# Optimization experiments

Hardware: AMD Instinct MI355X
Metric: run time of the kernel (lower is better)

## Reference

```python
import jax, jax.numpy as jnp
import numpy as np
from math import log2, floor

B, N, DIM = 2, 2048, 2048
HEADS, DIM_HEAD, FF_MULT = 16, 128, 4
RMS_EPS = 1e-8


def _get_slopes(heads):
    def pow2_slopes(n):
        start = 2 ** (-2 ** (-(log2(n) - 3)))
        return [start * start ** i for i in range(n)]
    if log2(heads).is_integer():
        return pow2_slopes(heads)
    closest = 2 ** floor(log2(heads))
    return pow2_slopes(closest) + pow2_slopes(2 * closest)[0::2][: heads - closest]


def setup_inputs() -> dict:
    key = jax.random.key(0)
    ks = jax.random.split(key, 5)
    std = 0.02
    return {
        "x": jax.random.normal(ks[0], (B, N, DIM), dtype=jnp.float32),
        "g": jnp.ones((DIM,), dtype=jnp.float32),
        "w_qkv": jax.random.normal(ks[1], (DIM, DIM + DIM_HEAD), dtype=jnp.float32) * std,
        "w_attn_out": jax.random.normal(ks[2], (DIM, DIM), dtype=jnp.float32) * std,
        "w_ff1": jax.random.normal(ks[3], (DIM, 2 * FF_MULT * DIM), dtype=jnp.float32) * std,
        "w_ff2": jax.random.normal(ks[4], (FF_MULT * DIM, DIM), dtype=jnp.float32) * std,
    }


def reference(x, g, w_qkv, w_attn_out, w_ff1, w_ff2):
    b, n, dim = x.shape
    # RMSNorm: x / clamp(||x|| * dim^-0.5, eps) * g
    norm = jnp.linalg.norm(x, axis=-1, keepdims=True) * (dim ** -0.5)
    xn = x / jnp.maximum(norm, RMS_EPS) * g

    # Parallel SwiGLU FFN branch (shares normed input with attention)
    h = xn @ w_ff1                       # [b, n, 2*ff_mult*dim]
    val, gate = jnp.split(h, 2, axis=-1)
    ff_out = (jax.nn.silu(gate) * val) @ w_ff2  # [b, n, dim]

    # Multi-query attention: single dim_head-wide kv shared as K and V
    qkv = xn @ w_qkv                     # [b, n, dim + dim_head]
    q, kv = qkv[..., :dim], qkv[..., dim:]
    q = q.reshape(b, n, HEADS, DIM_HEAD) * (DIM_HEAD ** -0.5)
    sim = jnp.einsum('bihd,bjd->bhij', q, kv)  # [b, h, n, n]

    # ALiBi bias: -|j - i| * slope_h
    slopes = jnp.asarray(_get_slopes(HEADS), dtype=sim.dtype)[:, None, None]
    pos = jnp.arange(n)
    bias = -jnp.abs(pos[None, None, :] - pos[None, :, None]).astype(sim.dtype) * slopes
    sim = sim + bias

    # Causal mask (strict upper triangle masked)
    causal = jnp.triu(jnp.ones((n, n), dtype=bool), 1)
    neg = jnp.asarray(jnp.finfo(sim.dtype).max, sim.dtype)
    sim = jnp.where(causal, -neg, sim)

    attn = jax.nn.softmax(sim, axis=-1)
    out = jnp.einsum('bhij,bjd->bhid', attn, kv)     # [b, h, n, dim_head]
    out = out.transpose(0, 2, 1, 3).reshape(b, n, dim)
    return out @ w_attn_out + ff_out
```

## Files before the change

kernel.cpp:

```cpp
#include <hip/hip_runtime.h>
#include <stdint.h>

typedef unsigned short u16;
typedef __attribute__((ext_vector_type(8))) short bf16x8;
typedef __attribute__((ext_vector_type(4))) float f32x4;
typedef __attribute__((ext_vector_type(8))) unsigned short us8;
typedef __attribute__((ext_vector_type(4))) float fvec4;

#define BATCH 2
#define SEQ   2048
#define DIMM  2048
#define NH    16
#define DH    128
#define ROWS  (BATCH*SEQ)
#define QKVN  (DIMM + DH)
#define FFH   8192
#define LOG2E 1.44269504088896340736f

static __device__ __forceinline__ u16 f2bf(float x) {
  union { float f; uint32_t u; } v; v.f = x;
  uint32_t r = (v.u + 0x7fffu + ((v.u >> 16) & 1u)) >> 16;
  return (u16)r;
}

static __device__ __forceinline__ float fast_exp2(float x) {
  float r; asm("v_exp_f32 %0, %1" : "=v"(r) : "v"(x)); return r;
}

static __device__ __forceinline__ void gld_lds16(const void* g, void* l) {
  __builtin_amdgcn_global_load_lds(
      (const __attribute__((address_space(1))) uint32_t*)g,
      (__attribute__((address_space(3))) uint32_t*)l, 16, 0, 0);
}

__global__ __launch_bounds__(256)
void rmsnorm_k(const float* __restrict__ x, const float* __restrict__ g, u16* __restrict__ xn) {
  const int row = blockIdx.x;
  const float* xr = x + (size_t)row * DIMM;
  const int off = threadIdx.x * 8;
  fvec4 a = *(const fvec4*)(xr + off);
  fvec4 b = *(const fvec4*)(xr + off + 4);
  float ss = a[0]*a[0]+a[1]*a[1]+a[2]*a[2]+a[3]*a[3]
           + b[0]*b[0]+b[1]*b[1]+b[2]*b[2]+b[3]*b[3];
  #pragma unroll
  for (int m = 32; m >= 1; m >>= 1) ss += __shfl_xor(ss, m);
  __shared__ float red[4];
  if ((threadIdx.x & 63) == 0) red[threadIdx.x >> 6] = ss;
  __syncthreads();
  float tot = red[0] + red[1] + red[2] + red[3];
  float inv = 1.0f / fmaxf(sqrtf(tot * (1.0f / DIMM)), 1e-8f);
  fvec4 ga = *(const fvec4*)(g + off);
  fvec4 gb = *(const fvec4*)(g + off + 4);
  us8 o;
  #pragma unroll
  for (int i = 0; i < 4; i++) { o[i] = f2bf(a[i]*inv*ga[i]); o[4+i] = f2bf(b[i]*inv*gb[i]); }
  *(us8*)(xn + (size_t)row * DIMM + off) = o;
}

template<typename TIN>
__global__ __launch_bounds__(256)
void transpose_to_bf16(const TIN* __restrict__ in, u16* __restrict__ out, int R, int C) {
  __shared__ u16 tile[64 * 65];
  const int r0 = blockIdx.y * 64, c0 = blockIdx.x * 64;
  const int tr = threadIdx.x >> 2;
  const int tc = (threadIdx.x & 3) * 16;
  const TIN* ip = in + (size_t)(r0 + tr) * C + c0 + tc;
  u16 tmp[16];
  #pragma unroll
  for (int i = 0; i < 16; i++) {
    if constexpr (sizeof(TIN) == 4) tmp[i] = f2bf(((const float*)ip)[i]);
    else                            tmp[i] = ((const u16*)ip)[i];
  }
  #pragma unroll
  for (int i = 0; i < 16; i++) tile[tr * 65 + tc + i] = tmp[i];
  __syncthreads();
  const int oc  = c0 + tr;
  const int orr = (threadIdx.x & 3) * 16;
  us8 v0, v1;
  #pragma unroll
  for (int i = 0; i < 8; i++) v0[i] = tile[(orr + i) * 65 + tr];
  #pragma unroll
  for (int i = 0; i < 8; i++) v1[i] = tile[(orr + 8 + i) * 65 + tr];
  u16* op = out + (size_t)oc * R + r0 + orr;
  *(us8*)op = v0;
  *(us8*)(op + 8) = v1;
}

template<int MODE>
__global__ __launch_bounds__(256, 2)
void gemm_bf16(const u16* __restrict__ A, const u16* __restrict__ BT, int K,
               float* __restrict__ outF, u16* __restrict__ outQ, u16* __restrict__ outKV) {
  __shared__ __align__(16) u16 lA[128 * 32];
  __shared__ __align__(16) u16 lB[128 * 32];
  const int tid = threadIdx.x;
  const int wave = tid >> 6, lane = tid & 63;
  const int lid = lane & 15, quad = lane >> 4;
  const int wm = wave >> 1, wn = wave & 1;
  const int row0 = blockIdx.y * 128;
  const int col0 = blockIdx.x * 128;
  f32x4 acc[4][4];
  #pragma unroll
  for (int i = 0; i < 4; i++)
    #pragma unroll
    for (int j = 0; j < 4; j++) { acc[i][j][0]=0.f; acc[i][j][1]=0.f; acc[i][j][2]=0.f; acc[i][j][3]=0.f; }

  const int rA0 = wave * 32;
  const int rsub = lane >> 2;
  const int cl = lane & 3;

  for (int k0 = 0; k0 < K; k0 += 32) {
    #pragma unroll
    for (int h2 = 0; h2 < 2; ++h2) {
      int rloc = rA0 + h2 * 16 + rsub;
      int gc = cl ^ ((rloc >> 1) & 3);
      gld_lds16(A  + (size_t)(row0 + rloc) * K + k0 + gc * 8, lA + (rA0 + h2 * 16) * 32);
      gld_lds16(BT + (size_t)(col0 + rloc) * K + k0 + gc * 8, lB + (rA0 + h2 * 16) * 32);
    }
    __syncthreads();
    bf16x8 af[4], bfr[4];
    #pragma unroll
    for (int i = 0; i < 4; i++) {
      int r  = wm * 64 + i * 16 + lid;
      af[i]  = *(const bf16x8*)(lA + r * 32 + (quad ^ ((r >> 1) & 3)) * 8);
      int rb = wn * 64 + i * 16 + lid;
      bfr[i] = *(const bf16x8*)(lB + rb * 32 + (quad ^ ((rb >> 1) & 3)) * 8);
    }
    #pragma unroll
    for (int im = 0; im < 4; im++)
      #pragma unroll
      for (int in = 0; in < 4; in++)
        acc[im][in] = __builtin_amdgcn_mfma_f32_16x16x32_bf16(af[im], bfr[in], acc[im][in], 0, 0, 0);
    __syncthreads();
  }

  #pragma unroll
  for (int im = 0; im < 4; im++)
    #pragma unroll
    for (int in = 0; in < 4; in++) {
      int col = col0 + wn * 64 + in * 16 + lid;
      int rbase = row0 + wm * 64 + im * 16 + quad * 4;
      #pragma unroll
      for (int rg = 0; rg < 4; rg++) {
        float v = acc[im][in][rg];
        int row = rbase + rg;
        if constexpr (MODE == 0) {
          if (col < DIMM) outQ[(size_t)row * DIMM + col] = f2bf(v);
          else            outKV[(size_t)row * DH + (col - DIMM)] = f2bf(v);
        } else if constexpr (MODE == 2) {
          outF[(size_t)row * DIMM + col] = v;
        } else {
          outF[(size_t)row * DIMM + col] += v;
        }
      }
    }
}

static __device__ __forceinline__ void stage_half(const u16* __restrict__ src, u16* dst,
                                                  int K, int sr, int sgc, int wave) {
  gld_lds16(src + (size_t)sr * K + sgc,       dst + wave * 1024);
  gld_lds16(src + (size_t)(sr + 8) * K + sgc, dst + wave * 1024 + 512);
}

static __device__ __forceinline__ void lda4(bf16x8 (&dst)[4][2], const u16* sAb,
                                            int mh, int wm, int lid, int c0) {
  #pragma unroll
  for (int i = 0; i < 4; ++i) {
    const u16* p = sAb + (mh * 128 + wm * 64 + i * 16 + lid) * 64;
    dst[i][0] = *(const bf16x8*)(p + c0);
    dst[i][1] = *(const bf16x8*)(p + (c0 ^ 32));
  }
}

static __device__ __forceinline__ void ldb2(bf16x8 (&dst)[2][2], const u16* sBb,
                                            int nh, int wn, int lid, int c0) {
  #pragma unroll
  for (int n = 0; n < 2; ++n) {
    const u16* p = sBb + (nh * 128 + wn * 32 + n * 16 + lid) * 64;
    dst[n][0] = *(const bf16x8*)(p + c0);
    dst[n][1] = *(const bf16x8*)(p + (c0 ^ 32));
  }
}

static __device__ __forceinline__ void quad16(f32x4 (&acc)[8][4], const bf16x8 (&af)[4][2],
                                              const bf16x8 (&bf)[2][2], int mh, int nh) {
  __builtin_amdgcn_s_setprio(1);
  #pragma unroll
  for (int i = 0; i < 4; ++i)
    #pragma unroll
    for (int n = 0; n < 2; ++n) {
      f32x4 c = acc[mh * 4 + i][nh * 2 + n];
      c = __builtin_amdgcn_mfma_f32_16x16x32_bf16(af[i][0], bf[n][0], c, 0, 0, 0);
      c = __builtin_amdgcn_mfma_f32_16x16x32_bf16(af[i][1], bf[n][1], c, 0, 0, 0);
      acc[mh * 4 + i][nh * 2 + n] = c;
    }
  __builtin_amdgcn_s_setprio(0);
}

__global__ __launch_bounds__(512, 2)
void gemm_ff1_swiglu_8p(const u16* __restrict__ A, const u16* __restrict__ BT,
                        u16* __restrict__ FF) {
  __shared__ __align__(16) u16 sA[2][256 * 64];
  __shared__ __align__(16) u16 sB[2][256 * 64];
  const int tid = threadIdx.x;
  const int wave = tid >> 6, lane = tid & 63;
  const int lid = lane & 15, quad = lane >> 4;
  const int wm = wave >> 2, wn = wave & 3;
  const int K = DIMM;

  int orig = blockIdx.y * 64 + blockIdx.x;
  int swz = (orig & 7) * 128 + (orig >> 3);
  const int row0 = (swz >> 6) * 256;
  const int n0 = (swz & 63) * 128;

  const int sr  = wave * 16 + (lane >> 3);
  const int sgc = (((lane & 7) ^ (lane >> 3)) << 3);
  const int c0  = ((quad ^ (lid & 7)) << 3);

  f32x4 acc[8][4];
  #pragma unroll
  for (int i = 0; i < 8; ++i)
    #pragma unroll
    for (int j = 0; j < 4; ++j) { acc[i][j][0]=0.f; acc[i][j][1]=0.f; acc[i][j][2]=0.f; acc[i][j][3]=0.f; }

  #define STAGE_A(b, h, kt) stage_half(A  + (size_t)(row0 + (h)*128) * K + (kt)*64, &sA[b][(h)*8192], K, sr, sgc, wave)
  #define STAGE_B(b, h, kt) stage_half(BT + (size_t)((h) ? (FFH + n0) : n0) * K + (kt)*64, &sB[b][(h)*8192], K, sr, sgc, wave)
  #define BAR() __builtin_amdgcn_s_barrier()

  STAGE_A(0, 0, 0); STAGE_A(0, 1, 0); STAGE_B(0, 0, 0); STAGE_B(0, 1, 0);
  STAGE_A(1, 0, 1); STAGE_B(1, 0, 1); STAGE_B(1, 1, 1);
  asm volatile("s_waitcnt vmcnt(6)" ::: "memory");
  BAR();

  const int niter = K / 128;
  for (int I = 0; I < niter; ++I) {
    const bool more = (I + 1 < niter);
    const int kt1 = 2 * I + 1, kt2 = 2 * I + 2, kt3 = 2 * I + 3;
    bf16x8 af[4][2], b0f[2][2], b1f[2][2];

    lda4(af, sA[0], 0, wm, lid, c0);
    ldb2(b0f, sB[0], 0, wn, lid, c0);
    STAGE_A(1, 1, kt1);
    BAR();
    quad16(acc, af, b0f, 0, 0);
    BAR();
    ldb2(b1f, sB[0], 1, wn, lid, c0);
    if (more) STAGE_A(0, 0, kt2);
    BAR();
    quad16(acc, af, b1f, 0, 1);
    BAR();
    lda4(af, sA[0], 1, wm, lid, c0);
    if (more) STAGE_B(0, 0, kt2);
    BAR();
    quad16(acc, af, b1f, 1, 1);
    BAR();
    if (more) STAGE_B(0, 1, kt2);
    BAR();
    quad16(acc, af, b0f, 1, 0);
    if (more) { asm volatile("s_waitcnt vmcnt(6)" ::: "memory"); }
    else      { asm volatile("s_waitcnt vmcnt(0)" ::: "memory"); }
    BAR();

    lda4(af, sA[1], 0, wm, lid, c0);
    ldb2(b0f, sB[1], 0, wn, lid, c0);
    if (more) STAGE_A(0, 1, kt2);
    BAR();
    quad16(acc, af, b0f, 0, 0);
    BAR();
    ldb2(b1f, sB[1], 1, wn, lid, c0);
    if (more) STAGE_A(1, 0, kt3);
    BAR();
    quad16(acc, af, b1f, 0, 1);
    BAR();
    lda4(af, sA[1], 1, wm, lid, c0);
    if (more) STAGE_B(1, 0, kt3);
    BAR();
    quad16(acc, af, b1f, 1, 1);
    BAR();
    if (more) STAGE_B(1, 1, kt3);
    BAR();
    quad16(acc, af, b0f, 1, 0);
    if (more) { asm volatile("s_waitcnt vmcnt(6)" ::: "memory"); }
    BAR();
  }

  #undef STAGE_A
  #undef STAGE_B
  #undef BAR

  #pragma unroll
  for (int mi = 0; mi < 8; ++mi) {
    const int row = row0 + (mi >> 2) * 128 + wm * 64 + (mi & 3) * 16 + quad * 4;
    #pragma unroll
    for (int n = 0; n < 2; ++n) {
      const int col = n0 + wn * 32 + n * 16 + lid;
      #pragma unroll
      for (int rg = 0; rg < 4; ++rg) {
        float vv = acc[mi][n][rg];
        float gg = acc[mi][2 + n][rg];
        float sig = 1.0f / (1.0f + fast_exp2(-gg * LOG2E));
        FF[(size_t)(row + rg) * FFH + col] = f2bf(vv * gg * sig);
      }
    }
  }
}

__global__ __launch_bounds__(256, 1)
void attn_k2(const u16* __restrict__ qws, const u16* __restrict__ kvws,
             const u16* __restrict__ kvt, u16* __restrict__ attnws) {
  __shared__ __align__(16) u16 kvls[128 * 128];
  __shared__ __align__(16) u16 kvtls[128 * 128];
  __shared__ __align__(16) u16 plds[4][32][136];
  const int tid = threadIdx.x;
  const int wave = tid >> 6, lane = tid & 63;
  const int lid = lane & 15, quad = lane >> 4;
  const int hb = blockIdx.y;
  const int h = hb & (NH - 1), b = hb >> 4;
  const int pair = blockIdx.x;
  const float slope2 = fast_exp2(-0.5f * (float)(h + 1)) * LOG2E;
  const float scale2 = 0.08838834764831845f * LOG2E;
  const float NEG = -__builtin_inff();

  const u16* kvb  = kvws + (size_t)b * SEQ * DH;
  const u16* kvtb = kvt  + (size_t)b * DH * SEQ;

  #pragma unroll 1
  for (int tt = 0; tt < 2; tt++) {
    const int T = tt ? (15 - pair) : pair;
    const int rw = T * 128 + wave * 32;

    bf16x8 qf[2][4];
    #pragma unroll
    for (int ig = 0; ig < 2; ig++)
      #pragma unroll
      for (int ks = 0; ks < 4; ks++)
        qf[ig][ks] = *(const bf16x8*)(qws + (size_t)(b * SEQ + rw + ig * 16 + lid) * DIMM
                                       + h * DH + ks * 32 + quad * 8);
    float srow2[2][4];
    #pragma unroll
    for (int ig = 0; ig < 2; ig++)
      #pragma unroll
      for (int rg = 0; rg < 4; rg++)
        srow2[ig][rg] = slope2 * (float)(rw + ig * 16 + quad * 4 + rg);

    f32x4 o[2][8];
    #pragma unroll
    for (int ig = 0; ig < 2; ig++)
      #pragma unroll
      for (int nd = 0; nd < 8; nd++) { o[ig][nd][0]=0.f; o[ig][nd][1]=0.f; o[ig][nd][2]=0.f; o[ig][nd][3]=0.f; }
    float m2[2][4], l[2][4];
    #pragma unroll
    for (int ig = 0; ig < 2; ig++)
      #pragma unroll
      for (int rg = 0; rg < 4; rg++) { m2[ig][rg] = NEG; l[ig][rg] = 0.f; }

    const int njt = T + 1;
    #pragma unroll 1
    for (int jt = 0; jt < njt; jt++) {
      const int j0 = jt * 128;
      __syncthreads();
      {
        const int c = lane & 15;
        const int r4 = lane >> 4;
        #pragma unroll
        for (int it = 0; it < 8; it++) {
          const int r = wave * 32 + it * 4 + r4;
          const int gc = c ^ (r & 15);
          gld_lds16(kvb  + (size_t)(j0 + r) * DH + gc * 8,        kvls  + (wave * 32 + it * 4) * 128);
          gld_lds16(kvtb + (size_t)r * SEQ + j0 + gc * 8,         kvtls + (wave * 32 + it * 4) * 128);
        }
      }
      __syncthreads();

      const int rhi = rw + 31;
      const int nbmax = min(8, ((rhi - j0) >> 4) + 1);
      const int ks2max = (nbmax + 1) >> 1;

      float pvv[2][8][4];
      float mt[2][4];
      #pragma unroll
      for (int ig = 0; ig < 2; ig++)
        #pragma unroll
        for (int rg = 0; rg < 4; rg++) mt[ig][rg] = NEG;

      #pragma unroll
      for (int nb = 0; nb < 8; nb++) {
        if (nb < nbmax) {
          bf16x8 bk[4];
          #pragma unroll
          for (int ks = 0; ks < 4; ks++)
            bk[ks] = *(const bf16x8*)(kvls + (nb * 16 + lid) * 128 + (((ks * 4 + quad) ^ lid) << 3));
          f32x4 s0, s1;
          s0[0]=0.f;s0[1]=0.f;s0[2]=0.f;s0[3]=0.f;
          s1[0]=0.f;s1[1]=0.f;s1[2]=0.f;s1[3]=0.f;
          #pragma unroll
          for (int ks = 0; ks < 4; ks++) {
            s0 = __builtin_amdgcn_mfma_f32_16x16x32_bf16(qf[0][ks], bk[ks], s0, 0, 0, 0);
            s1 = __builtin_amdgcn_mfma_f32_16x16x32_bf16(qf[1][ks], bk[ks], s1, 0, 0, 0);
          }
          const int jl = j0 + nb * 16 + lid;
          const float sj = slope2 * (float)jl;
          #pragma unroll
          for (int rg = 0; rg < 4; rg++) {
            const int row0r = rw + quad * 4 + rg;
            float e0 = fmaf(s0[rg], scale2, sj) - srow2[0][rg];
            e0 = (jl <= row0r) ? e0 : NEG;
            pvv[0][nb][rg] = e0;
            mt[0][rg] = fmaxf(mt[0][rg], e0);
            float e1 = fmaf(s1[rg], scale2, sj) - srow2[1][rg];
            e1 = (jl <= row0r + 16) ? e1 : NEG;
            pvv[1][nb][rg] = e1;
            mt[1][rg] = fmaxf(mt[1][rg], e1);
          }
        }
      }

      float alpha[2][4];
      #pragma unroll
      for (int ig = 0; ig < 2; ig++)
        #pragma unroll
        for (int rg = 0; rg < 4; rg++) {
          float m = mt[ig][rg];
          m = fmaxf(m, __shfl_xor(m, 1));
          m = fmaxf(m, __shfl_xor(m, 2));
          m = fmaxf(m, __shfl_xor(m, 4));
          m = fmaxf(m, __shfl_xor(m, 8));
          float mn = fmaxf(m2[ig][rg], m);
          alpha[ig][rg] = fast_exp2(m2[ig][rg] - mn);
          m2[ig][rg] = mn;
        }

      float rs[2][4];
      #pragma unroll
      for (int ig = 0; ig < 2; ig++)
        #pragma unroll
        for (int rg = 0; rg < 4; rg++) rs[ig][rg] = 0.f;
      #pragma unroll
      for (int nb = 0; nb < 8; nb++) {
        if (nb < nbmax) {
          #pragma unroll
          for (int ig = 0; ig < 2; ig++)
            #pragma unroll
            for (int rg = 0; rg < 4; rg++) {
              float p = fast_exp2(pvv[ig][nb][rg] - m2[ig][rg]);
              rs[ig][rg] += p;
              plds[wave][ig * 16 + quad * 4 + rg][nb * 16 + lid] = f2bf(p);
            }
        }
      }
      if (nbmax & 1) {
        #pragma unroll
        for (int ig = 0; ig < 2; ig++)
          #pragma unroll
          for (int rg = 0; rg < 4; rg++)
            plds[wave][ig * 16 + quad * 4 + rg][nbmax * 16 + lid] = 0;
      }

      #pragma unroll
      for (int ig = 0; ig < 2; ig++)
        #pragma unroll
        for (int rg = 0; rg < 4; rg++) {
          float r = rs[ig][rg];
          r += __shfl_xor(r, 1);
          r += __shfl_xor(r, 2);
          r += __shfl_xor(r, 4);
          r += __shfl_xor(r, 8);
          l[ig][rg] = l[ig][rg] * alpha[ig][rg] + r;
        }
      #pragma unroll
      for (int ig = 0; ig < 2; ig++)
        #pragma unroll
        for (int nd = 0; nd < 8; nd++)
          #pragma unroll
          for (int rg = 0; rg < 4; rg++) o[ig][nd][rg] *= alpha[ig][rg];

      asm volatile("s_waitcnt lgkmcnt(0)" ::: "memory");
      #pragma unroll
      for (int ks2 = 0; ks2 < 4; ks2++) {
        if (ks2 < ks2max) {
          bf16x8 pa0 = *(const bf16x8*)&plds[wave][lid][ks2 * 32 + quad * 8];
          bf16x8 pa1 = *(const bf16x8*)&plds[wave][16 + lid][ks2 * 32 + quad * 8];
          #pragma unroll
          for (int nd = 0; nd < 8; nd++) {
            bf16x8 bv = *(const bf16x8*)(kvtls + (nd * 16 + lid) * 128 + (((ks2 * 4 + quad) ^ lid) << 3));
            o[0][nd] = __builtin_amdgcn_mfma_f32_16x16x32_bf16(pa0, bv, o[0][nd], 0, 0, 0);
            o[1][nd] = __builtin_amdgcn_mfma_f32_16x16x32_bf16(pa1, bv, o[1][nd], 0, 0, 0);
          }
        }
      }
    }

    #pragma unroll
    for (int ig = 0; ig < 2; ig++) {
      float inv[4];
      #pragma unroll
      for (int rg = 0; rg < 4; rg++) inv[rg] = 1.0f / l[ig][rg];
      #pragma unroll
      for (int nd = 0; nd < 8; nd++)
        #pragma unroll
        for (int rg = 0; rg < 4; rg++) {
          int row = rw + ig * 16 + quad * 4 + rg;
          attnws[(size_t)(b * SEQ + row) * DIMM + h * DH + nd * 16 + lid] =
              f2bf(o[ig][nd][rg] * inv[rg]);
        }
    }
  }
}

extern "C" void kernel_launch(void* const* d_in, const int* in_sizes, int n_in,
                              void* d_out, int out_size, void* d_ws, size_t ws_size,
                              hipStream_t stream) {
  (void)in_sizes; (void)n_in; (void)out_size; (void)ws_size;
  const float* x     = (const float*)d_in[0];
  const float* g     = (const float*)d_in[1];
  const float* w_qkv = (const float*)d_in[2];
  const float* w_ao  = (const float*)d_in[3];
  const float* w_ff1 = (const float*)d_in[4];
  const float* w_ff2 = (const float*)d_in[5];
  float* out = (float*)d_out;

  u16* ws = (u16*)d_ws;
  u16* xn     = ws;
  u16* wTqkv  = xn     + 8388608;
  u16* wTattn = wTqkv  + 4456448;
  u16* wTff1  = wTattn + 4194304;
  u16* wTff2  = wTff1  + 33554432;
  u16* ffin   = wTff2  + 16777216;
  u16* qws    = ffin   + 33554432;
  u16* kvws   = qws    + 8388608;
  u16* kvtws  = kvws   + 524288;
  u16* attnws = kvtws  + 524288;

  transpose_to_bf16<float><<<dim3(QKVN/64, DIMM/64), 256, 0, stream>>>(w_qkv, wTqkv, DIMM, QKVN);
  transpose_to_bf16<float><<<dim3(DIMM/64, DIMM/64), 256, 0, stream>>>(w_ao, wTattn, DIMM, DIMM);
  transpose_to_bf16<float><<<dim3((2*FFH)/64, DIMM/64), 256, 0, stream>>>(w_ff1, wTff1, DIMM, 2*FFH);
  transpose_to_bf16<float><<<dim3(DIMM/64, FFH/64), 256, 0, stream>>>(w_ff2, wTff2, FFH, DIMM);

  rmsnorm_k<<<ROWS, 256, 0, stream>>>(x, g, xn);

  gemm_bf16<0><<<dim3(QKVN/128, ROWS/128), 256, 0, stream>>>(xn, wTqkv, DIMM, nullptr, qws, kvws);

  transpose_to_bf16<u16><<<dim3(DH/64, SEQ/64), 256, 0, stream>>>(kvws, kvtws, SEQ, DH);
  transpose_to_bf16<u16><<<dim3(DH/64, SEQ/64), 256, 0, stream>>>(kvws + (size_t)SEQ*DH, kvtws + (size_t)DH*SEQ, SEQ, DH);

  attn_k2<<<dim3(8, NH*BATCH), 256, 0, stream>>>(qws, kvws, kvtws, attnws);

  gemm_ff1_swiglu_8p<<<dim3(FFH/128, ROWS/256), 512, 0, stream>>>(xn, wTff1, ffin);
  gemm_bf16<2><<<dim3(DIMM/128, ROWS/128), 256, 0, stream>>>(ffin, wTff2, FFH, out, nullptr, nullptr);

  gemm_bf16<3><<<dim3(DIMM/128, ROWS/128), 256, 0, stream>>>(attnws, wTattn, DIMM, out, nullptr, nullptr);
}
```

Before: 1.004 ms.

## Use 256x256 eight-phase split-K kernel for FF2 and fold partials into attn-out

Replaces the FF2 GEMM, which used the generic 128x128 gemm_bf16 kernel, with a new 512-thread 256x256-tile kernel that shares the eight-phase LDS pipeline of the FF1 kernel. K is split in two, and the second partial goes into a scratch buffer that reuses the dead wTff1 region. The attention-output GEMM then adds that partial in its epilogue. The shared pipeline is pulled into a macro, and its vmcnt waits change from 6 to 10 with extra waits. This adds an extra fp32 partial write and read, and the wait counts must stay correct.

```diff
diff --git a/kernel.cpp b/kernel.cpp
--- a/kernel.cpp
+++ b/kernel.cpp
@@ -89,7 +89,8 @@
 template<int MODE>
 __global__ __launch_bounds__(256, 2)
 void gemm_bf16(const u16* __restrict__ A, const u16* __restrict__ BT, int K,
-               float* __restrict__ outF, u16* __restrict__ outQ, u16* __restrict__ outKV) {
+               float* __restrict__ outF, u16* __restrict__ outQ, u16* __restrict__ outKV,
+               const float* __restrict__ tmpF) {
   __shared__ __align__(16) u16 lA[128 * 32];
   __shared__ __align__(16) u16 lB[128 * 32];
   const int tid = threadIdx.x;
@@ -149,7 +150,8 @@
         } else if constexpr (MODE == 2) {
           outF[(size_t)row * DIMM + col] = v;
         } else {
-          outF[(size_t)row * DIMM + col] += v;
+          size_t idx = (size_t)row * DIMM + col;
+          outF[idx] += v + tmpF[idx];
         }
       }
     }
@@ -195,6 +197,74 @@
     }
   __builtin_amdgcn_s_setprio(0);
 }
+
+#define VMW(n) asm volatile("s_waitcnt vmcnt(" #n ")" ::: "memory")
+#define BAR8() __builtin_amdgcn_s_barrier()
+
+#define EIGHT_PHASE_LOOP(NITER)                                               \
+  {                                                                           \
+    STAGE_A(0,0,0); STAGE_B(0,0,0); STAGE_B(0,1,0); STAGE_A(0,1,0);           \
+    STAGE_A(1,0,1); STAGE_B(1,0,1); STAGE_B(1,1,1);                           \
+    VMW(10);                                                                  \
+    BAR8();                                                                   \
+    for (int I = 0; I < (NITER); ++I) {                                       \
+      const bool more = (I + 1 < (NITER));                                    \
+      const int kt1 = 2*I+1, kt2 = 2*I+2, kt3 = 2*I+3;                        \
+      bf16x8 af[4][2], b0f[2][2], b1f[2][2];                                  \
+                                                                      \
+      lda4(af, sA[0], 0, wm, lid, c0); ldb2(b0f, sB[0], 0, wn, lid, c0);      \
+      STAGE_A(1,1,kt1);                                                       \
+      BAR8();                                                                 \
+      quad16(acc, af, b0f, 0, 0);                                             \
+      if (more) { VMW(10); } else { VMW(0); }                                 \
+      BAR8();                                                                 \
+                                                                      \
+      ldb2(b1f, sB[0], 1, wn, lid, c0);                                       \
+      if (more) STAGE_A(0,0,kt2);                                             \
+      BAR8();                                                                 \
+      quad16(acc, af, b1f, 0, 1);                                             \
+      if (more) { VMW(10); }                                                  \
+      BAR8();                                                                 \
+                                                                      \
+      lda4(af, sA[0], 1, wm, lid, c0);                                        \
+      if (more) STAGE_B(0,0,kt2);                                             \
+      BAR8();                                                                 \
+      quad16(acc, af, b1f, 1, 1);                                             \
+      BAR8();                                                                 \
+                                                                      \
+      if (more) STAGE_B(0,1,kt2);                                             \
+      BAR8();                                                                 \
+      quad16(acc, af, b0f, 1, 0);                                             \
+      if (more) { VMW(10); }                                                  \
+      BAR8();                                                                 \
+                                                                      \
+      lda4(af, sA[1], 0, wm, lid, c0); ldb2(b0f, sB[1], 0, wn, lid, c0);      \
+      if (more) STAGE_A(0,1,kt2);                                             \
+      BAR8();                                                                 \
+      quad16(acc, af, b0f, 0, 0);                                             \
+      if (more) { VMW(10); }                                                  \
+      BAR8();                                                                 \
+                                                                      \
+      ldb2(b1f, sB[1], 1, wn, lid, c0);                                       \
+      if (more) STAGE_A(1,0,kt3);                                             \
+      BAR8();                                                                 \
+      quad16(acc, af, b1f, 0, 1);                                             \
+      if (more) { VMW(10); }                                                  \
+      BAR8();                                                                 \
+                                                                      \
+      lda4(af, sA[1], 1, wm, lid, c0);                                        \
+      if (more) STAGE_B(1,0,kt3);                                             \
+      BAR8();                                                                 \
+      quad16(acc, af, b1f, 1, 1);                                             \
+      BAR8();                                                                 \
+                                                                      \
+      if (more) STAGE_B(1,1,kt3);                                             \
+      BAR8();                                                                 \
+      quad16(acc, af, b0f, 1, 0);                                             \
+      if (more) { VMW(10); }                                                  \
+      BAR8();                                                                 \
+    }                                                                         \
+  }
 
 __global__ __launch_bounds__(512, 2)
 void gemm_ff1_swiglu_8p(const u16* __restrict__ A, const u16* __restrict__ BT,
@@ -224,68 +294,11 @@
 
   #define STAGE_A(b, h, kt) stage_half(A  + (size_t)(row0 + (h)*128) * K + (kt)*64, &sA[b][(h)*8192], K, sr, sgc, wave)
   #define STAGE_B(b, h, kt) stage_half(BT + (size_t)((h) ? (FFH + n0) : n0) * K + (kt)*64, &sB[b][(h)*8192], K, sr, sgc, wave)
-  #define BAR() __builtin_amdgcn_s_barrier()
-
-  STAGE_A(0, 0, 0); STAGE_A(0, 1, 0); STAGE_B(0, 0, 0); STAGE_B(0, 1, 0);
-  STAGE_A(1, 0, 1); STAGE_B(1, 0, 1); STAGE_B(1, 1, 1);
-  asm volatile("s_waitcnt vmcnt(6)" ::: "memory");
-  BAR();
-
-  const int niter = K / 128;
-  for (int I = 0; I < niter; ++I) {
-    const bool more = (I + 1 < niter);
-    const int kt1 = 2 * I + 1, kt2 = 2 * I + 2, kt3 = 2 * I + 3;
-    bf16x8 af[4][2], b0f[2][2], b1f[2][2];
-
-    lda4(af, sA[0], 0, wm, lid, c0);
-    ldb2(b0f, sB[0], 0, wn, lid, c0);
-    STAGE_A(1, 1, kt1);
-    BAR();
-    quad16(acc, af, b0f, 0, 0);
-    BAR();
-    ldb2(b1f, sB[0], 1, wn, lid, c0);
-    if (more) STAGE_A(0, 0, kt2);
-    BAR();
-    quad16(acc, af, b1f, 0, 1);
-    BAR();
-    lda4(af, sA[0], 1, wm, lid, c0);
-    if (more) STAGE_B(0, 0, kt2);
-    BAR();
-    quad16(acc, af, b1f, 1, 1);
-    BAR();
-    if (more) STAGE_B(0, 1, kt2);
-    BAR();
-    quad16(acc, af, b0f, 1, 0);
-    if (more) { asm volatile("s_waitcnt vmcnt(6)" ::: "memory"); }
-    else      { asm volatile("s_waitcnt vmcnt(0)" ::: "memory"); }
-    BAR();
-
-    lda4(af, sA[1], 0, wm, lid, c0);
-    ldb2(b0f, sB[1], 0, wn, lid, c0);
-    if (more) STAGE_A(0, 1, kt2);
-    BAR();
-    quad16(acc, af, b0f, 0, 0);
-    BAR();
-    ldb2(b1f, sB[1], 1, wn, lid, c0);
-    if (more) STAGE_A(1, 0, kt3);
-    BAR();
-    quad16(acc, af, b1f, 0, 1);
-    BAR();
-    lda4(af, sA[1], 1, wm, lid, c0);
-    if (more) STAGE_B(1, 0, kt3);
-    BAR();
-    quad16(acc, af, b1f, 1, 1);
-    BAR();
-    if (more) STAGE_B(1, 1, kt3);
-    BAR();
-    quad16(acc, af, b0f, 1, 0);
-    if (more) { asm volatile("s_waitcnt vmcnt(6)" ::: "memory"); }
-    BAR();
-  }
+
+  EIGHT_PHASE_LOOP(K / 128)
 
   #undef STAGE_A
   #undef STAGE_B
-  #undef BAR
 
   #pragma unroll
   for (int mi = 0; mi < 8; ++mi) {
@@ -300,6 +313,58 @@
         float sig = 1.0f / (1.0f + fast_exp2(-gg * LOG2E));
         FF[(size_t)(row + rg) * FFH + col] = f2bf(vv * gg * sig);
       }
+    }
+  }
+}
+
+__global__ __launch_bounds__(512, 2)
+void gemm_ff2_8p(const u16* __restrict__ A, const u16* __restrict__ BT,
+                 float* __restrict__ out0, float* __restrict__ out1) {
+  __shared__ __align__(16) u16 sA[2][256 * 64];
+  __shared__ __align__(16) u16 sB[2][256 * 64];
+  const int tid = threadIdx.x;
+  const int wave = tid >> 6, lane = tid & 63;
+  const int lid = lane & 15, quad = lane >> 4;
+  const int wm = wave >> 2, wn = wave & 3;
+  const int K = FFH;
+
+  int orig = (blockIdx.z * 16 + blockIdx.y) * 8 + blockIdx.x;
+  int swz = (orig & 7) * 32 + (orig >> 3);
+  const int n0   = (swz & 7) * 256;
+  const int ks   = (swz >> 3) & 1;
+  const int row0 = (swz >> 4) * 256;
+
+  const u16* Ab = A  + ks * 4096;
+  const u16* Bb = BT + ks * 4096;
+
+  const int sr  = wave * 16 + (lane >> 3);
+  const int sgc = (((lane & 7) ^ (lane >> 3)) << 3);
+  const int c0  = ((quad ^ (lid & 7)) << 3);
+
+  f32x4 acc[8][4];
+  #pragma unroll
+  for (int i = 0; i < 8; ++i)
+    #pragma unroll
+    for (int j = 0; j < 4; ++j) { acc[i][j][0]=0.f; acc[i][j][1]=0.f; acc[i][j][2]=0.f; acc[i][j][3]=0.f; }
+
+  #define STAGE_A(b, h, kt) stage_half(Ab + (size_t)(row0 + (h)*128) * K + (kt)*64, &sA[b][(h)*8192], K, sr, sgc, wave)
+  #define STAGE_B(b, h, kt) stage_half(Bb + (size_t)(n0 + (h)*128) * K + (kt)*64,  &sB[b][(h)*8192], K, sr, sgc, wave)
+
+  EIGHT_PHASE_LOOP(32)
+
+  #undef STAGE_A
+  #undef STAGE_B
+
+  float* dst = ks ? out1 : out0;
+  #pragma unroll
+  for (int mi = 0; mi < 8; ++mi) {
+    const int row = row0 + (mi >> 2) * 128 + wm * 64 + (mi & 3) * 16 + quad * 4;
+    #pragma unroll
+    for (int j = 0; j < 4; ++j) {
+      const int col = n0 + (j >> 1) * 128 + wn * 32 + (j & 1) * 16 + lid;
+      #pragma unroll
+      for (int rg = 0; rg < 4; ++rg)
+        dst[(size_t)(row + rg) * DIMM + col] = acc[mi][j][rg];
     }
   }
 }
@@ -529,6 +594,7 @@
   u16* kvws   = qws    + 8388608;
   u16* kvtws  = kvws   + 524288;
   u16* attnws = kvtws  + 524288;
+  float* tmpf = (float*)wTff1;
 
   transpose_to_bf16<float><<<dim3(QKVN/64, DIMM/64), 256, 0, stream>>>(w_qkv, wTqkv, DIMM, QKVN);
   transpose_to_bf16<float><<<dim3(DIMM/64, DIMM/64), 256, 0, stream>>>(w_ao, wTattn, DIMM, DIMM);
@@ -537,7 +603,7 @@
 
   rmsnorm_k<<<ROWS, 256, 0, stream>>>(x, g, xn);
 
-  gemm_bf16<0><<<dim3(QKVN/128, ROWS/128), 256, 0, stream>>>(xn, wTqkv, DIMM, nullptr, qws, kvws);
+  gemm_bf16<0><<<dim3(QKVN/128, ROWS/128), 256, 0, stream>>>(xn, wTqkv, DIMM, nullptr, qws, kvws, nullptr);
 
   transpose_to_bf16<u16><<<dim3(DH/64, SEQ/64), 256, 0, stream>>>(kvws, kvtws, SEQ, DH);
   transpose_to_bf16<u16><<<dim3(DH/64, SEQ/64), 256, 0, stream>>>(kvws + (size_t)SEQ*DH, kvtws + (size_t)DH*SEQ, SEQ, DH);
@@ -545,7 +611,7 @@
   attn_k2<<<dim3(8, NH*BATCH), 256, 0, stream>>>(qws, kvws, kvtws, attnws);
 
   gemm_ff1_swiglu_8p<<<dim3(FFH/128, ROWS/256), 512, 0, stream>>>(xn, wTff1, ffin);
-  gemm_bf16<2><<<dim3(DIMM/128, ROWS/128), 256, 0, stream>>>(ffin, wTff2, FFH, out, nullptr, nullptr);
-
-  gemm_bf16<3><<<dim3(DIMM/128, ROWS/128), 256, 0, stream>>>(attnws, wTattn, DIMM, out, nullptr, nullptr);
-}
+  gemm_ff2_8p<<<dim3(8, 16, 2), 512, 0, stream>>>(ffin, wTff2, out, tmpf);
+
+  gemm_bf16<3><<<dim3(DIMM/128, ROWS/128), 256, 0, stream>>>(attnws, wTattn, DIMM, out, nullptr, nullptr, tmpf);
+}
```

Measured after the change: 966.1 us. 1.04x faster.
